# Kernel optimization log

Hardware: AMD Instinct MI355X
Metric: run time of the kernel (lower is better)

Reference implementation:

```python
import jax, jax.numpy as jnp
import numpy as np

HIDDEN = 1024
N_HEAD = 16
HEAD_DIM = HIDDEN // N_HEAD
ROPE_THETA = 10000.0


def setup_inputs() -> dict:
    key = jax.random.key(0)
    ks = jax.random.split(key, 6)
    B, T = 4, 2048
    x = jax.random.normal(ks[0], (B, T, HIDDEN), dtype=jnp.float32)
    rnn_state = jax.random.normal(ks[1], (B, HIDDEN), dtype=jnp.float32)
    Wqkv = jax.random.normal(ks[2], (HIDDEN, 3 * HIDDEN), dtype=jnp.float32) * 0.02
    bqkv = jnp.zeros((3 * HIDDEN,), dtype=jnp.float32)
    Wproj = jax.random.normal(ks[3], (HIDDEN, HIDDEN), dtype=jnp.float32) * 0.02
    bproj = jnp.zeros((HIDDEN,), dtype=jnp.float32)
    return {"x": x, "rnn_state": rnn_state, "Wqkv": Wqkv, "bqkv": bqkv,
            "Wproj": Wproj, "bproj": bproj}


def _rope_tables(T, dtype):
    # GPT-NeoX style half-split RoPE
    inv_freq = 1.0 / (ROPE_THETA ** (jnp.arange(0, HEAD_DIM, 2, dtype=jnp.float32) / HEAD_DIM))
    freqs = jnp.arange(T, dtype=jnp.float32)[:, None] * inv_freq[None, :]  # [T, D/2]
    return jnp.cos(freqs).astype(dtype), jnp.sin(freqs).astype(dtype)


def _apply_rope(x, cos, sin):
    # x: [B, H, T, D]; cos/sin: [T, D/2]
    x1, x2 = jnp.split(x, 2, axis=-1)
    c = cos[None, None, :, :]
    s = sin[None, None, :, :]
    return jnp.concatenate([x1 * c - x2 * s, x1 * s + x2 * c], axis=-1)


def reference(x, rnn_state, Wqkv, bqkv, Wproj, bproj):
    B, T, C = x.shape
    qkv = x @ Wqkv + bqkv  # [B, T, 3C]
    q, k, v = jnp.split(qkv, 3, axis=-1)
    # split heads -> [B, H, T, D]
    def heads(t):
        return t.reshape(B, T, N_HEAD, HEAD_DIM).transpose(0, 2, 1, 3)
    q, k, v = heads(q), heads(k), heads(v)
    cos, sin = _rope_tables(T, x.dtype)
    q = _apply_rope(q, cos, sin)
    k = _apply_rope(k, cos, sin)
    scale = 1.0 / jnp.sqrt(jnp.asarray(HEAD_DIM, dtype=x.dtype))
    scores = jnp.einsum('bhtd,bhsd->bhts', q, k) * scale  # [B,H,T,T]
    # causal additive mask: 0 on/below diag, -inf above (matches torch buffer)
    causal = jnp.tril(jnp.ones((T, T), dtype=bool))
    scores = jnp.where(causal[None, None, :, :], scores, -jnp.inf)
    attn = jax.nn.softmax(scores, axis=-1)
    out = jnp.einsum('bhts,bhsd->bhtd', attn, v)  # [B,H,T,D]
    out = out.transpose(0, 2, 1, 3).reshape(B, T, C)
    output = out @ Wproj + bproj
    return (output, rnn_state)
```

## Files before the change

### kernel.cpp

```cpp
#include <hip/hip_runtime.h>
#include <cstdint>
#include <cstddef>
#include <math.h>

typedef unsigned short u16;
typedef __attribute__((ext_vector_type(8))) short short8;
typedef __attribute__((ext_vector_type(4))) float floatx4;

#define HIDDEN 1024
#define NHEAD 16
#define HD 64
#define BB 4
#define TT 2048
#define MM (BB*TT)
#define NQKV 3072
#define NEGINF (-30000.0f)

__device__ inline u16 f2bf(float f){
  union { float f; unsigned u; } v; v.f = f;
  unsigned r = v.u + 0x7FFFu + ((v.u >> 16) & 1u);
  return (u16)(r >> 16);
}
__device__ inline void load_lds16(const void* g, void* l){
  __builtin_amdgcn_global_load_lds((const __attribute__((address_space(1))) void*)g,
                                   (__attribute__((address_space(3))) void*)l,
                                   16, 0, 0);
}

__global__ void rope_tables(float* __restrict__ cosT, float* __restrict__ sinT){
  const int idx = blockIdx.x * 256 + threadIdx.x;
  const int t = idx >> 5, f = idx & 31;
  const float inv = powf(10000.0f, -(float)f * (1.0f / 32.0f));
  const float ang = (float)t * inv;
  cosT[idx] = cosf(ang);
  sinT[idx] = sinf(ang);
}

__global__ void convert_x(const float* __restrict__ in, u16* __restrict__ outp){
  const int i = (blockIdx.x * 256 + threadIdx.x) * 8;
  #pragma unroll
  for (int u = 0; u < 8; u++) outp[i + u] = f2bf(in[i + u]);
}

__global__ void transpose_f32_bf16(const float* __restrict__ in, u16* __restrict__ out,
                                   int R, int C){
  __shared__ alignas(16) u16 tile[32][33];
  const int c0 = blockIdx.x * 32, r0 = blockIdx.y * 32;
  const int tx = threadIdx.x & 31, ty = threadIdx.x >> 5;
  for (int i = ty; i < 32; i += 8)
    tile[i][tx] = f2bf(in[(size_t)(r0 + i) * C + c0 + tx]);
  __syncthreads();
  for (int i = ty; i < 32; i += 8) out[(size_t)(c0 + i) * R + r0 + tx] = tile[tx][i];
}

__global__ void gemm_qkv(const u16* __restrict__ X, const u16* __restrict__ WT,
                         const float* __restrict__ bias,
                         const float* __restrict__ ropeC, const float* __restrict__ ropeS,
                         u16* __restrict__ Qb, u16* __restrict__ Kb, u16* __restrict__ Vtg)
{
  __shared__ alignas(16) u16 As[128 * 32];
  __shared__ alignas(16) u16 Bs[128 * 32];
  __shared__ alignas(16) u16 VTx[4][64 * 24];
  const int tid = threadIdx.x;
  const int wid = tid >> 6, lane = tid & 63;
  const int quad = lane >> 4, ln = lane & 15;
  const int row0 = blockIdx.y * 128, col0 = blockIdx.x * 128;
  const int wm = (wid >> 1) * 64, wn = (wid & 1) * 64;
  floatx4 acc[4][4] = {};

  const int sr = tid >> 2, sk = (tid & 3) * 8;

  for (int kk = 0; kk < 32; ++kk){
    const int k0 = kk * 32;
    __syncthreads();
    load_lds16(&X [(size_t)(row0 + sr      ) * 1024 + k0 + sk], &As[(size_t)(tid      ) * 8]);
    load_lds16(&X [(size_t)(row0 + sr + 64 ) * 1024 + k0 + sk], &As[(size_t)(tid + 256) * 8]);
    load_lds16(&WT[(size_t)(col0 + sr      ) * 1024 + k0 + sk], &Bs[(size_t)(tid      ) * 8]);
    load_lds16(&WT[(size_t)(col0 + sr + 64 ) * 1024 + k0 + sk], &Bs[(size_t)(tid + 256) * 8]);
    __syncthreads();
    short8 a[4], b[4];
    #pragma unroll
    for (int i = 0; i < 4; i++) a[i] = *(const short8*)&As[(wm + i*16 + ln) * 32 + quad * 8];
    #pragma unroll
    for (int j = 0; j < 4; j++) b[j] = *(const short8*)&Bs[(wn + j*16 + ln) * 32 + quad * 8];
    #pragma unroll
    for (int i = 0; i < 4; i++)
      #pragma unroll
      for (int j = 0; j < 4; j++)
        acc[i][j] = __builtin_amdgcn_mfma_f32_16x16x32_bf16(a[i], b[j], acc[i][j], 0, 0, 0);
  }

  const int wcol0 = col0 + wn;
  const int which = wcol0 >> 10;
  const int h = (wcol0 & 1023) >> 6;
  float bs[4];
  #pragma unroll
  for (int j = 0; j < 4; j++) bs[j] = bias[wcol0 + j*16 + ln];

  if (which < 2){
    #pragma unroll
    for (int i = 0; i < 4; i++){
      #pragma unroll
      for (int rr = 0; rr < 4; rr++){
        const int rowg = row0 + wm + i*16 + quad*4 + rr;
        const int b_ = rowg >> 11, t = rowg & 2047;
        u16* op = (which == 0 ? Qb : Kb) + ((size_t)(b_ * NHEAD + h) * TT + t) * HD;
        #pragma unroll
        for (int j = 0; j < 2; j++){
          const int f = j*16 + ln;
          const float cs = ropeC[t * 32 + f];
          const float sn = ropeS[t * 32 + f];
          const float x1 = acc[i][j  ][rr] + bs[j  ];
          const float x2 = acc[i][j+2][rr] + bs[j+2];
          float y1 = x1 * cs - x2 * sn;
          float y2 = x1 * sn + x2 * cs;
          if (which == 0){ y1 *= 0.125f; y2 *= 0.125f; }
          op[f]      = f2bf(y1);
          op[f + 32] = f2bf(y2);
        }
      }
    }
  } else {
    #pragma unroll
    for (int i = 0; i < 4; i++){
      #pragma unroll
      for (int j = 0; j < 4; j++)
        #pragma unroll
        for (int rr = 0; rr < 4; rr++)
          VTx[wid][(j*16 + ln) * 24 + quad*4 + rr] = f2bf(acc[i][j][rr] + bs[j]);
      asm volatile("s_waitcnt lgkmcnt(0)" ::: "memory");
      const int d = lane;
      const short8 v0 = *(const short8*)&VTx[wid][d * 24 + 0];
      const short8 v1 = *(const short8*)&VTx[wid][d * 24 + 8];
      const int rowg = row0 + wm + i*16;
      const int b_ = rowg >> 11, t0 = rowg & 2047;
      u16* vp = &Vtg[((size_t)(b_ * NHEAD + h) * HD + d) * TT + t0];
      *(short8*)&vp[0] = v0;
      *(short8*)&vp[8] = v1;
      asm volatile("s_waitcnt lgkmcnt(0)" ::: "memory");
    }
  }
}

__global__ void attn(const u16* __restrict__ Qb, const u16* __restrict__ Kb,
                     const u16* __restrict__ Vtg, u16* __restrict__ AO)
{
  const int bh = blockIdx.x, tbi = 31 - (int)blockIdx.y;
  const int tid = threadIdx.x;
  const int wid = tid >> 6, lane = tid & 63;
  const int quad = lane >> 4, ln = lane & 15;

  __shared__ alignas(16) u16 Kl[64 * 72];
  __shared__ alignas(16) u16 Vt[64 * 72];
  __shared__ alignas(16) u16 Pl[4][16 * 72];

  const u16* Qh = Qb  + (size_t)bh * TT * HD;
  const u16* Kh = Kb  + (size_t)bh * TT * HD;
  const u16* Vh = Vtg + (size_t)bh * HD * TT;
  const int b_ = bh >> 4, h = bh & 15;

  const int q0 = tbi * 64 + wid * 16;

  const short8 aq0 = *(const short8*)&Qh[(size_t)(q0 + ln) * HD + quad*8];
  const short8 aq1 = *(const short8*)&Qh[(size_t)(q0 + ln) * HD + 32 + quad*8];

  floatx4 o[4] = {};
  float l_i[4] = {};

  const int nch = tbi + 1;
  for (int ch = 0; ch < nch; ++ch){
    const int key0 = ch * 64;
    __syncthreads();
    #pragma unroll
    for (int it = 0; it < 2; ++it){
      const int idx = it * 256 + tid;
      const int r = idx >> 3, c8 = (idx & 7) * 8;
      *(short8*)&Kl[r * 72 + c8] = *(const short8*)&Kh[(size_t)(key0 + r) * HD + c8];
      *(short8*)&Vt[r * 72 + c8] = *(const short8*)&Vh[(size_t)r * TT + key0 + c8];
    }
    __syncthreads();

    floatx4 s[4];
    #pragma unroll
    for (int j = 0; j < 4; j++){
      const short8 kb0 = *(const short8*)&Kl[(j*16 + ln) * 72 + quad*8];
      const short8 kb1 = *(const short8*)&Kl[(j*16 + ln) * 72 + 32 + quad*8];
      floatx4 z = {0.0f, 0.0f, 0.0f, 0.0f};
      z = __builtin_amdgcn_mfma_f32_16x16x32_bf16(aq0, kb0, z, 0, 0, 0);
      z = __builtin_amdgcn_mfma_f32_16x16x32_bf16(aq1, kb1, z, 0, 0, 0);
      s[j] = z;
    }
    if (ch == nch - 1){
      #pragma unroll
      for (int j = 0; j < 4; j++)
        #pragma unroll
        for (int rr = 0; rr < 4; rr++){
          const int key = key0 + j*16 + ln;
          const int t   = q0 + quad*4 + rr;
          if (key > t) s[j][rr] = NEGINF;
        }
    }
    #pragma unroll
    for (int j = 0; j < 4; j++)
      #pragma unroll
      for (int rr = 0; rr < 4; rr++){
        const float p = __expf(s[j][rr]);
        s[j][rr] = p;
        l_i[rr] += p;
      }
    #pragma unroll
    for (int j = 0; j < 4; j++)
      #pragma unroll
      for (int rr = 0; rr < 4; rr++)
        Pl[wid][(quad*4 + rr) * 72 + j*16 + ln] = f2bf(s[j][rr]);
    const short8 pa0 = *(const short8*)&Pl[wid][ln * 72 + quad*8];
    const short8 pa1 = *(const short8*)&Pl[wid][ln * 72 + 32 + quad*8];
    #pragma unroll
    for (int n = 0; n < 4; n++){
      const short8 vb0 = *(const short8*)&Vt[(n*16 + ln) * 72 + quad*8];
      const short8 vb1 = *(const short8*)&Vt[(n*16 + ln) * 72 + 32 + quad*8];
      o[n] = __builtin_amdgcn_mfma_f32_16x16x32_bf16(pa0, vb0, o[n], 0, 0, 0);
      o[n] = __builtin_amdgcn_mfma_f32_16x16x32_bf16(pa1, vb1, o[n], 0, 0, 0);
    }
  }

  #pragma unroll
  for (int rr = 0; rr < 4; rr++){
    float rs = l_i[rr];
    #pragma unroll
    for (int off = 1; off < 16; off <<= 1) rs += __shfl_xor(rs, off);
    l_i[rr] = rs;
  }

  #pragma unroll
  for (int n = 0; n < 4; n++)
    #pragma unroll
    for (int rr = 0; rr < 4; rr++){
      const int t = q0 + quad*4 + rr;
      const float inv_l = 1.0f / fmaxf(l_i[rr], 1e-20f);
      AO[(size_t)(b_ * TT + t) * HIDDEN + h * HD + n*16 + ln] = f2bf(o[n][rr] * inv_l);
    }
}

__global__ void gemm_proj(const u16* __restrict__ A, const u16* __restrict__ WT,
                          const float* __restrict__ bias, float* __restrict__ out)
{
  __shared__ alignas(16) u16 As[128 * 32];
  __shared__ alignas(16) u16 Bs[128 * 32];
  const int tid = threadIdx.x;
  const int wid = tid >> 6, lane = tid & 63;
  const int quad = lane >> 4, ln = lane & 15;
  const int row0 = blockIdx.y * 128, col0 = blockIdx.x * 128;
  const int wm = (wid >> 1) * 64, wn = (wid & 1) * 64;
  floatx4 acc[4][4] = {};

  const int sr = tid >> 2, sk = (tid & 3) * 8;

  for (int kk = 0; kk < 32; ++kk){
    const int k0 = kk * 32;
    __syncthreads();
    load_lds16(&A [(size_t)(row0 + sr      ) * 1024 + k0 + sk], &As[(size_t)(tid      ) * 8]);
    load_lds16(&A [(size_t)(row0 + sr + 64 ) * 1024 + k0 + sk], &As[(size_t)(tid + 256) * 8]);
    load_lds16(&WT[(size_t)(col0 + sr      ) * 1024 + k0 + sk], &Bs[(size_t)(tid      ) * 8]);
    load_lds16(&WT[(size_t)(col0 + sr + 64 ) * 1024 + k0 + sk], &Bs[(size_t)(tid + 256) * 8]);
    __syncthreads();
    short8 a[4], b[4];
    #pragma unroll
    for (int i = 0; i < 4; i++) a[i] = *(const short8*)&As[(wm + i*16 + ln) * 32 + quad * 8];
    #pragma unroll
    for (int j = 0; j < 4; j++) b[j] = *(const short8*)&Bs[(wn + j*16 + ln) * 32 + quad * 8];
    #pragma unroll
    for (int i = 0; i < 4; i++)
      #pragma unroll
      for (int j = 0; j < 4; j++)
        acc[i][j] = __builtin_amdgcn_mfma_f32_16x16x32_bf16(a[i], b[j], acc[i][j], 0, 0, 0);
  }

  float bs[4];
  #pragma unroll
  for (int j = 0; j < 4; j++) bs[j] = bias[col0 + wn + j*16 + ln];
  #pragma unroll
  for (int i = 0; i < 4; i++)
    #pragma unroll
    for (int rr = 0; rr < 4; rr++){
      const int rowg = row0 + wm + i*16 + quad*4 + rr;
      #pragma unroll
      for (int j = 0; j < 4; j++)
        out[(size_t)rowg * HIDDEN + col0 + wn + j*16 + ln] = acc[i][j][rr] + bs[j];
    }
}

__global__ void copy_tail(const float* __restrict__ rnn, float* __restrict__ out){
  const int i = blockIdx.x * 256 + threadIdx.x;
  if (i < BB * HIDDEN) out[(size_t)MM * HIDDEN + i] = rnn[i];
}

extern "C" void kernel_launch(void* const* d_in, const int* in_sizes, int n_in,
                              void* d_out, int out_size, void* d_ws, size_t ws_size,
                              hipStream_t stream)
{
  const float* x     = (const float*)d_in[0];
  const float* rnn   = (const float*)d_in[1];
  const float* Wqkv  = (const float*)d_in[2];
  const float* bqkv  = (const float*)d_in[3];
  const float* Wproj = (const float*)d_in[4];
  const float* bproj = (const float*)d_in[5];
  float* out = (float*)d_out;

  char* ws = (char*)d_ws;
  size_t off = 0;
  float* ropeC  = (float*)(ws + off); off += (size_t)TT * 32 * 4;
  float* ropeS  = (float*)(ws + off); off += (size_t)TT * 32 * 4;
  u16*   xN     = (u16*)(ws + off);   off += (size_t)MM * HIDDEN * 2;
  u16*   WqkvT  = (u16*)(ws + off);   off += (size_t)NQKV * HIDDEN * 2;
  u16*   WprojT = (u16*)(ws + off);   off += (size_t)HIDDEN * HIDDEN * 2;
  u16*   Qb     = (u16*)(ws + off);   off += (size_t)MM * HIDDEN * 2;
  u16*   Kb     = (u16*)(ws + off);   off += (size_t)MM * HIDDEN * 2;
  u16*   Vtg    = (u16*)(ws + off);   off += (size_t)MM * HIDDEN * 2;
  u16*   AO     = (u16*)(ws + off);   off += (size_t)MM * HIDDEN * 2;

  rope_tables<<<(TT * 32) / 256, 256, 0, stream>>>(ropeC, ropeS);
  convert_x<<<(MM * HIDDEN) / (256 * 8), 256, 0, stream>>>(x, xN);
  transpose_f32_bf16<<<dim3(NQKV / 32, HIDDEN / 32), 256, 0, stream>>>(Wqkv, WqkvT, HIDDEN, NQKV);
  transpose_f32_bf16<<<dim3(HIDDEN / 32, HIDDEN / 32), 256, 0, stream>>>(Wproj, WprojT, HIDDEN, HIDDEN);
  gemm_qkv<<<dim3(NQKV / 128, MM / 128), 256, 0, stream>>>(xN, WqkvT, bqkv, ropeC, ropeS, Qb, Kb, Vtg);
  attn<<<dim3(BB * NHEAD, 32), 256, 0, stream>>>(Qb, Kb, Vtg, AO);
  gemm_proj<<<dim3(HIDDEN / 128, MM / 128), 256, 0, stream>>>(AO, WprojT, bproj, out);
  copy_tail<<<(BB * HIDDEN + 255) / 256, 256, 0, stream>>>(rnn, out);
}
```

Before: 274.8 us.

## Process 128 queries per attention block with two query tiles per wave

Each attention block now covers 128 query rows instead of 64, with every wave handling two 16-row query tiles that reuse each loaded K/V chunk from shared memory. The grid's query dimension is halved and per-wave chunks that lie entirely above the causal diagonal are skipped, with the mask applied only on diagonal tiles. This halves the global K/V loads per query and amortises the LDS traffic. In exchange each wave uses more registers, there are half as many blocks, and waves within a block have uneven causal work, which can hurt occupancy and load balance.

```diff
diff --git a/kernel.cpp b/kernel.cpp
--- a/kernel.cpp
+++ b/kernel.cpp
@@ -145,29 +145,33 @@
 __global__ void attn(const u16* __restrict__ Qb, const u16* __restrict__ Kb,
                      const u16* __restrict__ Vtg, u16* __restrict__ AO)
 {
-  const int bh = blockIdx.x, tbi = 31 - (int)blockIdx.y;
+  const int bh = blockIdx.x, tbi = 15 - (int)blockIdx.y;
   const int tid = threadIdx.x;
   const int wid = tid >> 6, lane = tid & 63;
   const int quad = lane >> 4, ln = lane & 15;
 
   __shared__ alignas(16) u16 Kl[64 * 72];
   __shared__ alignas(16) u16 Vt[64 * 72];
-  __shared__ alignas(16) u16 Pl[4][16 * 72];
+  __shared__ alignas(16) u16 Pl[4][2][16 * 72];
 
   const u16* Qh = Qb  + (size_t)bh * TT * HD;
   const u16* Kh = Kb  + (size_t)bh * TT * HD;
   const u16* Vh = Vtg + (size_t)bh * HD * TT;
   const int b_ = bh >> 4, h = bh & 15;
 
-  const int q0 = tbi * 64 + wid * 16;
-
-  const short8 aq0 = *(const short8*)&Qh[(size_t)(q0 + ln) * HD + quad*8];
-  const short8 aq1 = *(const short8*)&Qh[(size_t)(q0 + ln) * HD + 32 + quad*8];
-
-  floatx4 o[4] = {};
-  float l_i[4] = {};
-
-  const int nch = tbi + 1;
+  const int qbase = tbi * 128 + wid * 32;
+
+  short8 aq[2][2];
+  #pragma unroll
+  for (int qt = 0; qt < 2; qt++){
+    aq[qt][0] = *(const short8*)&Qh[(size_t)(qbase + qt*16 + ln) * HD + quad*8];
+    aq[qt][1] = *(const short8*)&Qh[(size_t)(qbase + qt*16 + ln) * HD + 32 + quad*8];
+  }
+
+  floatx4 o[2][4] = {};
+  float l_i[2][4] = {};
+
+  const int nch = 2 * (tbi + 1);
   for (int ch = 0; ch < nch; ++ch){
     const int key0 = ch * 64;
     __syncthreads();
@@ -180,66 +184,72 @@
     }
     __syncthreads();
 
-    floatx4 s[4];
-    #pragma unroll
-    for (int j = 0; j < 4; j++){
-      const short8 kb0 = *(const short8*)&Kl[(j*16 + ln) * 72 + quad*8];
-      const short8 kb1 = *(const short8*)&Kl[(j*16 + ln) * 72 + 32 + quad*8];
-      floatx4 z = {0.0f, 0.0f, 0.0f, 0.0f};
-      z = __builtin_amdgcn_mfma_f32_16x16x32_bf16(aq0, kb0, z, 0, 0, 0);
-      z = __builtin_amdgcn_mfma_f32_16x16x32_bf16(aq1, kb1, z, 0, 0, 0);
-      s[j] = z;
-    }
-    if (ch == nch - 1){
-      #pragma unroll
-      for (int j = 0; j < 4; j++)
+    if (key0 <= qbase + 31){
+      #pragma unroll
+      for (int j = 0; j < 4; j++){
+        const short8 kb0 = *(const short8*)&Kl[(j*16 + ln) * 72 + quad*8];
+        const short8 kb1 = *(const short8*)&Kl[(j*16 + ln) * 72 + 32 + quad*8];
         #pragma unroll
-        for (int rr = 0; rr < 4; rr++){
-          const int key = key0 + j*16 + ln;
-          const int t   = q0 + quad*4 + rr;
-          if (key > t) s[j][rr] = NEGINF;
+        for (int qt = 0; qt < 2; qt++){
+          const int qt0 = qbase + qt*16;
+          floatx4 z = {0.0f, 0.0f, 0.0f, 0.0f};
+          z = __builtin_amdgcn_mfma_f32_16x16x32_bf16(aq[qt][0], kb0, z, 0, 0, 0);
+          z = __builtin_amdgcn_mfma_f32_16x16x32_bf16(aq[qt][1], kb1, z, 0, 0, 0);
+          if (key0 + 63 > qt0){
+            #pragma unroll
+            for (int rr = 0; rr < 4; rr++){
+              const int key = key0 + j*16 + ln;
+              const int t   = qt0 + quad*4 + rr;
+              if (key > t) z[rr] = NEGINF;
+            }
+          }
+          #pragma unroll
+          for (int rr = 0; rr < 4; rr++){
+            const float p = __expf(z[rr]);
+            l_i[qt][rr] += p;
+            Pl[wid][qt][(quad*4 + rr) * 72 + j*16 + ln] = f2bf(p);
+          }
         }
-    }
-    #pragma unroll
-    for (int j = 0; j < 4; j++)
+      }
+      short8 pa0[2], pa1[2];
+      #pragma unroll
+      for (int qt = 0; qt < 2; qt++){
+        pa0[qt] = *(const short8*)&Pl[wid][qt][ln * 72 + quad*8];
+        pa1[qt] = *(const short8*)&Pl[wid][qt][ln * 72 + 32 + quad*8];
+      }
+      #pragma unroll
+      for (int n = 0; n < 4; n++){
+        const short8 vb0 = *(const short8*)&Vt[(n*16 + ln) * 72 + quad*8];
+        const short8 vb1 = *(const short8*)&Vt[(n*16 + ln) * 72 + 32 + quad*8];
+        #pragma unroll
+        for (int qt = 0; qt < 2; qt++){
+          o[qt][n] = __builtin_amdgcn_mfma_f32_16x16x32_bf16(pa0[qt], vb0, o[qt][n], 0, 0, 0);
+          o[qt][n] = __builtin_amdgcn_mfma_f32_16x16x32_bf16(pa1[qt], vb1, o[qt][n], 0, 0, 0);
+        }
+      }
+    }
+  }
+
+  #pragma unroll
+  for (int qt = 0; qt < 2; qt++)
+    #pragma unroll
+    for (int rr = 0; rr < 4; rr++){
+      float rs = l_i[qt][rr];
+      #pragma unroll
+      for (int off = 1; off < 16; off <<= 1) rs += __shfl_xor(rs, off);
+      l_i[qt][rr] = rs;
+    }
+
+  #pragma unroll
+  for (int qt = 0; qt < 2; qt++)
+    #pragma unroll
+    for (int n = 0; n < 4; n++)
       #pragma unroll
       for (int rr = 0; rr < 4; rr++){
-        const float p = __expf(s[j][rr]);
-        s[j][rr] = p;
-        l_i[rr] += p;
-      }
-    #pragma unroll
-    for (int j = 0; j < 4; j++)
-      #pragma unroll
-      for (int rr = 0; rr < 4; rr++)
-        Pl[wid][(quad*4 + rr) * 72 + j*16 + ln] = f2bf(s[j][rr]);
-    const short8 pa0 = *(const short8*)&Pl[wid][ln * 72 + quad*8];
-    const short8 pa1 = *(const short8*)&Pl[wid][ln * 72 + 32 + quad*8];
-    #pragma unroll
-    for (int n = 0; n < 4; n++){
-      const short8 vb0 = *(const short8*)&Vt[(n*16 + ln) * 72 + quad*8];
-      const short8 vb1 = *(const short8*)&Vt[(n*16 + ln) * 72 + 32 + quad*8];
-      o[n] = __builtin_amdgcn_mfma_f32_16x16x32_bf16(pa0, vb0, o[n], 0, 0, 0);
-      o[n] = __builtin_amdgcn_mfma_f32_16x16x32_bf16(pa1, vb1, o[n], 0, 0, 0);
-    }
-  }
-
-  #pragma unroll
-  for (int rr = 0; rr < 4; rr++){
-    float rs = l_i[rr];
-    #pragma unroll
-    for (int off = 1; off < 16; off <<= 1) rs += __shfl_xor(rs, off);
-    l_i[rr] = rs;
-  }
-
-  #pragma unroll
-  for (int n = 0; n < 4; n++)
-    #pragma unroll
-    for (int rr = 0; rr < 4; rr++){
-      const int t = q0 + quad*4 + rr;
-      const float inv_l = 1.0f / fmaxf(l_i[rr], 1e-20f);
-      AO[(size_t)(b_ * TT + t) * HIDDEN + h * HD + n*16 + ln] = f2bf(o[n][rr] * inv_l);
-    }
+        const int t = qbase + qt*16 + quad*4 + rr;
+        const float inv_l = 1.0f / fmaxf(l_i[qt][rr], 1e-20f);
+        AO[(size_t)(b_ * TT + t) * HIDDEN + h * HD + n*16 + ln] = f2bf(o[qt][n][rr] * inv_l);
+      }
 }
 
 __global__ void gemm_proj(const u16* __restrict__ A, const u16* __restrict__ WT,
@@ -324,7 +334,7 @@
   transpose_f32_bf16<<<dim3(NQKV / 32, HIDDEN / 32), 256, 0, stream>>>(Wqkv, WqkvT, HIDDEN, NQKV);
   transpose_f32_bf16<<<dim3(HIDDEN / 32, HIDDEN / 32), 256, 0, stream>>>(Wproj, WprojT, HIDDEN, HIDDEN);
   gemm_qkv<<<dim3(NQKV / 128, MM / 128), 256, 0, stream>>>(xN, WqkvT, bqkv, ropeC, ropeS, Qb, Kb, Vtg);
-  attn<<<dim3(BB * NHEAD, 32), 256, 0, stream>>>(Qb, Kb, Vtg, AO);
+  attn<<<dim3(BB * NHEAD, 16), 256, 0, stream>>>(Qb, Kb, Vtg, AO);
   gemm_proj<<<dim3(HIDDEN / 128, MM / 128), 256, 0, stream>>>(AO, WprojT, bproj, out);
   copy_tail<<<(BB * HIDDEN + 255) / 256, 256, 0, stream>>>(rnn, out);
 }
```

Result: no change. 270.6 us (-1.5%).
